# Optimization experiments

Measured on AMD Instinct MI355X. Metric: run time of the kernel, lower is better.

Reference implementation:

```python
import jax, jax.numpy as jnp
import numpy as np

BS, N, C_IMG, C_PT, H, W = 8, 100000, 512, 256, 48, 160


def setup_inputs() -> dict:
    key = jax.random.key(0)
    ks = jax.random.split(key, 8)
    point_feat = jax.random.normal(ks[0], (N, C_PT), dtype=jnp.float32)
    # pillar centers in LiDAR frame: x forward [10,60], y left [-10,10], z [-2,1]
    u = jax.random.uniform(ks[1], (N, 3), dtype=jnp.float32)
    pillar_centers = jnp.stack([
        10.0 + 50.0 * u[:, 0],
        -10.0 + 20.0 * u[:, 1],
        -2.0 + 3.0 * u[:, 2],
    ], axis=1)
    batch_idx = jax.random.randint(ks[2], (N,), 0, BS, dtype=jnp.int32)
    img_feat = jax.random.normal(ks[3], (BS, C_IMG, H, W), dtype=jnp.float32)
    # KITTI-style calibration (per batch, small jitter)
    f, cx, cy = 80.0, 80.0, 24.0
    P2_base = np.array([[f, 0, cx, 0], [0, f, cy, 0], [0, 0, 1, 0]], dtype=np.float32)
    Tr_base = np.array([[0, -1, 0, 0], [0, 0, -1, 0], [1, 0, 0, 0], [0, 0, 0, 1]], dtype=np.float32)
    rng = np.random.RandomState(0)
    P2 = np.stack([P2_base + 0.01 * rng.randn(3, 4).astype(np.float32) for _ in range(BS)])
    R0 = np.stack([np.eye(4, dtype=np.float32) for _ in range(BS)])
    Tr = np.stack([Tr_base + 0.001 * rng.randn(4, 4).astype(np.float32) for _ in range(BS)])
    align_w = jax.random.normal(ks[4], (C_PT, C_IMG), dtype=jnp.float32) * 0.02
    align_b = jax.random.normal(ks[5], (C_PT,), dtype=jnp.float32) * 0.02
    return {
        'point_feat': point_feat, 'pillar_centers': pillar_centers,
        'img_feat': img_feat, 'P2': jnp.asarray(P2), 'R0': jnp.asarray(R0),
        'Tr': jnp.asarray(Tr), 'align_w': align_w, 'align_b': align_b,
        'batch_idx': batch_idx, 'img_h': H, 'img_w': W,
    }


def _fuse(point_feat, pillar_centers, img_feat, P2, R0, Tr, align_w, align_b,
          batch_idx, img_h, img_w):
    n = point_feat.shape[0]
    dt = point_feat.dtype
    # --- project_to_image (vectorized over all points via per-point calib gather) ---
    pts_hom = jnp.concatenate([pillar_centers, jnp.ones((n, 1), dtype=dt)], axis=1)  # [N,4]
    pts_cam = jnp.einsum('nij,nj->ni', Tr[batch_idx], pts_hom)    # [N,4]
    pts_rect = jnp.einsum('nij,nj->ni', R0[batch_idx], pts_cam)   # [N,4]
    pts_img = jnp.einsum('nij,nj->ni', P2[batch_idx], pts_rect)   # [N,3]
    depth = jnp.clip(pts_img[:, 2:3], 1e-5, None)
    uv = pts_img[:, :2] / depth
    valid = ((pts_img[:, 2] > 0) & (uv[:, 0] >= 0) & (uv[:, 0] < img_w)
             & (uv[:, 1] >= 0) & (uv[:, 1] < img_h))
    # --- grid_sample bilinear, align_corners=True, padding_mode='zeros' ---
    # grid = 2*uv/(dim-1)-1 with align_corners=True => pixel coords == uv.
    _, C, Hf, Wf = img_feat.shape
    u_, v_ = uv[:, 0], uv[:, 1]
    x0 = jnp.floor(u_); y0 = jnp.floor(v_)
    wx1 = u_ - x0; wx0 = 1.0 - wx1
    wy1 = v_ - y0; wy0 = 1.0 - wy1

    def gather(xi, yi):
        inb = (xi >= 0) & (xi <= Wf - 1) & (yi >= 0) & (yi <= Hf - 1)
        xc = jnp.clip(xi, 0, Wf - 1).astype(jnp.int32)
        yc = jnp.clip(yi, 0, Hf - 1).astype(jnp.int32)
        f = img_feat[batch_idx, :, yc, xc]  # [N,C]
        return f * inb.astype(dt)[:, None]

    sampled = (gather(x0, y0) * (wx0 * wy0)[:, None]
               + gather(x0 + 1, y0) * (wx1 * wy0)[:, None]
               + gather(x0, y0 + 1) * (wx0 * wy1)[:, None]
               + gather(x0 + 1, y0 + 1) * (wx1 * wy1)[:, None])
    sampled = jnp.where(valid[:, None], sampled, jnp.zeros((), dtype=dt))
    # --- align (Linear) + residual add ---
    aligned = sampled @ align_w.T + align_b
    return point_feat + aligned


def reference(point_feat, pillar_centers, img_feat, P2, R0, Tr, align_w, align_b,
              batch_idx, img_h, img_w):
    return _fuse(point_feat, pillar_centers, img_feat, P2, R0, Tr,
                 align_w, align_b, batch_idx, img_h, img_w)
```

## Files before the change

### kernel.cpp

```cpp
#include <hip/hip_runtime.h>

#define C_IMG 512
#define C_PT  256
#define IMG_H 48
#define IMG_W 160
#define HWPIX (IMG_H * IMG_W)

#define MP   64
#define BK   64
#define SPAD 72

typedef short bf16x8 __attribute__((ext_vector_type(8)));
typedef float f32x4  __attribute__((ext_vector_type(4)));
typedef unsigned u32x4 __attribute__((ext_vector_type(4)));

static __device__ __forceinline__ unsigned short f2bf(float f) {
    unsigned u = __float_as_uint(f);
    u += 0x7fffu + ((u >> 16) & 1u);
    return (unsigned short)(u >> 16);
}
static __device__ __forceinline__ unsigned pack2(float lo, float hi) {
    return (unsigned)f2bf(lo) | ((unsigned)f2bf(hi) << 16);
}
static __device__ __forceinline__ unsigned short f2bf_hu(float f) {
    return (unsigned short)((__float_as_uint(f) + 0x8000u) >> 16);
}
static __device__ __forceinline__ unsigned pack2_hu(float lo, float hi) {
    return ((__float_as_uint(lo) + 0x8000u) >> 16)
         | ((__float_as_uint(hi) + 0x8000u) & 0xffff0000u);
}
static __device__ __forceinline__ float bflo(unsigned v) { return __uint_as_float(v << 16); }
static __device__ __forceinline__ float bfhi(unsigned v) { return __uint_as_float(v & 0xffff0000u); }

__global__ __launch_bounds__(256)
void cvt_w_kernel(const float* __restrict__ alw, unsigned short* __restrict__ alwT) {
    const int i = (blockIdx.x * 256 + threadIdx.x) * 8;
    const float4 a = *(const float4*)(alw + i);
    const float4 b = *(const float4*)(alw + i + 4);
    uint4 o;
    o.x = pack2(a.x, a.y); o.y = pack2(a.z, a.w);
    o.z = pack2(b.x, b.y); o.w = pack2(b.z, b.w);
    *(uint4*)(alwT + i) = o;
}

__global__ __launch_bounds__(256)
void params_kernel(const float* __restrict__ centers,
                   const float* __restrict__ P2,
                   const float* __restrict__ R0,
                   const float* __restrict__ Tr,
                   const int*   __restrict__ bidx,
                   u32x4* __restrict__ poff,
                   f32x4* __restrict__ pwgt,
                   int n)
{
    const int p = blockIdx.x * 256 + threadIdx.x;
    if (p >= n) return;
    const float cx = centers[p * 3 + 0];
    const float cy = centers[p * 3 + 1];
    const float cz = centers[p * 3 + 2];
    const int   b  = bidx[p];
    const float* tr = Tr + b * 16;
    const float c0 = tr[0]*cx + tr[1]*cy + tr[2]*cz + tr[3];
    const float c1 = tr[4]*cx + tr[5]*cy + tr[6]*cz + tr[7];
    const float c2 = tr[8]*cx + tr[9]*cy + tr[10]*cz + tr[11];
    const float c3 = tr[12]*cx + tr[13]*cy + tr[14]*cz + tr[15];
    const float* r0 = R0 + b * 16;
    const float e0 = r0[0]*c0 + r0[1]*c1 + r0[2]*c2 + r0[3]*c3;
    const float e1 = r0[4]*c0 + r0[5]*c1 + r0[6]*c2 + r0[7]*c3;
    const float e2 = r0[8]*c0 + r0[9]*c1 + r0[10]*c2 + r0[11]*c3;
    const float e3 = r0[12]*c0 + r0[13]*c1 + r0[14]*c2 + r0[15]*c3;
    const float* p2 = P2 + b * 12;
    const float ix = p2[0]*e0 + p2[1]*e1 + p2[2]*e2  + p2[3]*e3;
    const float iy = p2[4]*e0 + p2[5]*e1 + p2[6]*e2  + p2[7]*e3;
    const float iz = p2[8]*e0 + p2[9]*e1 + p2[10]*e2 + p2[11]*e3;
    const float depth = fmaxf(iz, 1e-5f);
    const float u = ix / depth;
    const float v = iy / depth;
    const bool valid = (iz > 0.f) && (u >= 0.f) && (u < (float)IMG_W)
                                 && (v >= 0.f) && (v < (float)IMG_H);
    const float x0f = floorf(u), y0f = floorf(v);
    const float wx1 = u - x0f, wx0 = 1.f - wx1;
    const float wy1 = v - y0f, wy0 = 1.f - wy1;
    const float cwv[4] = {wx0 * wy0, wx1 * wy0, wx0 * wy1, wx1 * wy1};
    f32x4 wg; u32x4 of;
    #pragma unroll
    for (int j = 0; j < 4; ++j) {
        const float xf = x0f + (float)(j & 1);
        const float yf = y0f + (float)(j >> 1);
        const bool inb = (xf >= 0.f) && (xf <= (float)(IMG_W - 1))
                      && (yf >= 0.f) && (yf <= (float)(IMG_H - 1));
        const int xc = (int)fminf(fmaxf(xf, 0.f), (float)(IMG_W - 1));
        const int yc = (int)fminf(fmaxf(yf, 0.f), (float)(IMG_H - 1));
        wg[j] = (valid && inb) ? cwv[j] : 0.f;
        of[j] = (unsigned)(((b * IMG_H + yc) * IMG_W + xc) * C_PT);
    }
    poff[p] = of;
    pwgt[p] = wg;
}

__global__ __launch_bounds__(256)
void proj_kernel(const float* __restrict__ img,
                 const unsigned short* __restrict__ wbf,
                 unsigned short* __restrict__ PT)
{
    __shared__ float sF[2][64][68];
    const int blk  = blockIdx.x;
    const int b    = blk / (HWPIX / 64);
    const int hw0  = (blk % (HWPIX / 64)) * 64;
    const int tid  = threadIdx.x;
    const int lane = tid & 63;
    const int wid  = tid >> 6;
    const int l15  = lane & 15;
    const int quad = lane >> 4;

    const int sr   = tid >> 2;
    const int scc  = tid & 3;
    const int sdst = ((scc ^ ((sr >> 3) & 3)) << 4);
    const float* gsrc = img + (size_t)b * C_IMG * HWPIX + hw0 + scc * 16;

    f32x4 acc[4][4];
    #pragma unroll
    for (int i = 0; i < 4; ++i)
        #pragma unroll
        for (int j = 0; j < 4; ++j)
            acc[i][j] = (f32x4){0.f, 0.f, 0.f, 0.f};

    const unsigned short* bw = wbf + (size_t)(wid * 64 + l15) * C_IMG + quad * 8;

    float4 st[4];
    {
        const float* gp = gsrc + (size_t)sr * HWPIX;
        #pragma unroll
        for (int k = 0; k < 4; ++k) st[k] = *(const float4*)(gp + 4 * k);
        #pragma unroll
        for (int k = 0; k < 4; ++k) *(float4*)&sF[0][sr][sdst + 4 * k] = st[k];
    }
    __syncthreads();

    for (int ck = 0; ck < C_IMG / 64; ++ck) {
        const int cur = ck & 1;
        if (ck < C_IMG / 64 - 1) {
            const float* gp = gsrc + (size_t)((ck + 1) * 64 + sr) * HWPIX;
            #pragma unroll
            for (int k = 0; k < 4; ++k) st[k] = *(const float4*)(gp + 4 * k);
        }
        #pragma unroll
        for (int kk = 0; kk < 2; ++kk) {
            bf16x8 af[4], bfr[4];
            #pragma unroll
            for (int nt = 0; nt < 4; ++nt)
                bfr[nt] = *(const bf16x8*)(bw + (size_t)(nt * 16) * C_IMG + ck * 64 + kk * 32);
            const int rbase = kk * 32 + quad * 8;
            #pragma unroll
            for (int mt = 0; mt < 4; ++mt) {
                const int col = ((mt ^ quad) << 4) + l15;
                float f[8];
                #pragma unroll
                for (int j = 0; j < 8; ++j) f[j] = sF[cur][rbase + j][col];
                union { unsigned u[4]; bf16x8 v; } cv;
                #pragma unroll
                for (int w2 = 0; w2 < 4; ++w2)
                    cv.u[w2] = pack2_hu(f[2 * w2], f[2 * w2 + 1]);
                af[mt] = cv.v;
            }
            #pragma unroll
            for (int mt = 0; mt < 4; ++mt)
                #pragma unroll
                for (int nt = 0; nt < 4; ++nt)
                    acc[mt][nt] = __builtin_amdgcn_mfma_f32_16x16x32_bf16(
                        af[mt], bfr[nt], acc[mt][nt], 0, 0, 0);
        }
        if (ck < C_IMG / 64 - 1) {
            #pragma unroll
            for (int k = 0; k < 4; ++k) *(float4*)&sF[cur ^ 1][sr][sdst + 4 * k] = st[k];
        }
        __syncthreads();
    }

    #pragma unroll
    for (int mt = 0; mt < 4; ++mt) {
        #pragma unroll
        for (int r = 0; r < 4; ++r) {
            const int pix = mt * 16 + quad * 4 + r;
            unsigned short* dst = PT + (size_t)(b * HWPIX + hw0 + pix) * C_PT + wid * 64 + l15;
            #pragma unroll
            for (int nt = 0; nt < 4; ++nt)
                dst[nt * 16] = f2bf_hu(acc[mt][nt][r]);
        }
    }
}

__global__ __launch_bounds__(256)
void point_kernel(const float* __restrict__ pf,
                  const unsigned short* __restrict__ PT,
                  const float* __restrict__ alb,
                  const u32x4* __restrict__ poff,
                  const f32x4* __restrict__ pwgt,
                  float* __restrict__ out,
                  int n)
{
    const int tid  = threadIdx.x;
    const int lane = tid & 63;
    const int wid  = tid >> 6;
    const int sub  = lane >> 5;
    const int ch0  = (lane & 31) * 8;
    const int base = blockIdx.x * 32 + wid * 8 + sub;

    const f32x4 ab0 = *(const f32x4*)(alb + ch0);
    const f32x4 ab1 = *(const f32x4*)(alb + ch0 + 4);

    #pragma unroll
    for (int it = 0; it < 4; ++it) {
        const int p = base + it * 2;
        if (p < n) {
            const u32x4 of = poff[p];
            const f32x4 wg = pwgt[p];
            float s0 = 0.f, s1 = 0.f, s2 = 0.f, s3 = 0.f;
            float s4 = 0.f, s5 = 0.f, s6 = 0.f, s7 = 0.f;
            #pragma unroll
            for (int j = 0; j < 4; ++j) {
                const u32x4 g = *(const u32x4*)(PT + of[j] + ch0);
                const float w = wg[j];
                s0 = fmaf(w, bflo(g[0]), s0); s1 = fmaf(w, bfhi(g[0]), s1);
                s2 = fmaf(w, bflo(g[1]), s2); s3 = fmaf(w, bfhi(g[1]), s3);
                s4 = fmaf(w, bflo(g[2]), s4); s5 = fmaf(w, bfhi(g[2]), s5);
                s6 = fmaf(w, bflo(g[3]), s6); s7 = fmaf(w, bfhi(g[3]), s7);
            }
            const size_t idx = (size_t)p * C_PT + ch0;
            const f32x4 a  = __builtin_nontemporal_load((const f32x4*)(pf + idx));
            const f32x4 b4 = __builtin_nontemporal_load((const f32x4*)(pf + idx + 4));
            f32x4 o0, o1;
            o0[0] = a[0] + ab0[0] + s0;  o0[1] = a[1] + ab0[1] + s1;
            o0[2] = a[2] + ab0[2] + s2;  o0[3] = a[3] + ab0[3] + s3;
            o1[0] = b4[0] + ab1[0] + s4; o1[1] = b4[1] + ab1[1] + s5;
            o1[2] = b4[2] + ab1[2] + s6; o1[3] = b4[3] + ab1[3] + s7;
            __builtin_nontemporal_store(o0, (f32x4*)(out + idx));
            __builtin_nontemporal_store(o1, (f32x4*)(out + idx + 4));
        }
    }
}

__global__ __launch_bounds__(256)
void fused_fallback_kernel(const float* __restrict__ pf,
                           const float* __restrict__ centers,
                           const float* __restrict__ img,
                           const float* __restrict__ P2,
                           const float* __restrict__ R0,
                           const float* __restrict__ Tr,
                           const float* __restrict__ alw,
                           const float* __restrict__ alb,
                           const int*   __restrict__ bidx,
                           float* __restrict__ out,
                           int n)
{
    __shared__ float          sWg[MP][4];
    __shared__ int            sOf[MP][4];
    __shared__ unsigned short sS[MP][SPAD];
    __shared__ unsigned short sW[C_PT][SPAD];

    const int tid = threadIdx.x;
    const int pt0 = blockIdx.x * MP;

    if (tid < MP) {
        const int p = pt0 + tid;
        float w[4] = {0.f, 0.f, 0.f, 0.f};
        int   o[4] = {0, 0, 0, 0};
        if (p < n) {
            const float cx = centers[p * 3 + 0];
            const float cy = centers[p * 3 + 1];
            const float cz = centers[p * 3 + 2];
            const int   b  = bidx[p];
            const float* tr = Tr + b * 16;
            const float c0 = tr[0]*cx + tr[1]*cy + tr[2]*cz + tr[3];
            const float c1 = tr[4]*cx + tr[5]*cy + tr[6]*cz + tr[7];
            const float c2 = tr[8]*cx + tr[9]*cy + tr[10]*cz + tr[11];
            const float c3 = tr[12]*cx + tr[13]*cy + tr[14]*cz + tr[15];
            const float* r0 = R0 + b * 16;
            const float e0 = r0[0]*c0 + r0[1]*c1 + r0[2]*c2 + r0[3]*c3;
            const float e1 = r0[4]*c0 + r0[5]*c1 + r0[6]*c2 + r0[7]*c3;
            const float e2 = r0[8]*c0 + r0[9]*c1 + r0[10]*c2 + r0[11]*c3;
            const float e3 = r0[12]*c0 + r0[13]*c1 + r0[14]*c2 + r0[15]*c3;
            const float* p2 = P2 + b * 12;
            const float ix = p2[0]*e0 + p2[1]*e1 + p2[2]*e2  + p2[3]*e3;
            const float iy = p2[4]*e0 + p2[5]*e1 + p2[6]*e2  + p2[7]*e3;
            const float iz = p2[8]*e0 + p2[9]*e1 + p2[10]*e2 + p2[11]*e3;
            const float depth = fmaxf(iz, 1e-5f);
            const float u = ix / depth;
            const float v = iy / depth;
            const bool valid = (iz > 0.f) && (u >= 0.f) && (u < (float)IMG_W)
                                         && (v >= 0.f) && (v < (float)IMG_H);
            const float x0f = floorf(u), y0f = floorf(v);
            const float wx1 = u - x0f, wx0 = 1.f - wx1;
            const float wy1 = v - y0f, wy0 = 1.f - wy1;
            const float cwv[4] = {wx0 * wy0, wx1 * wy0, wx0 * wy1, wx1 * wy1};
            #pragma unroll
            for (int j = 0; j < 4; ++j) {
                const float xf = x0f + (float)(j & 1);
                const float yf = y0f + (float)(j >> 1);
                const bool inb = (xf >= 0.f) && (xf <= (float)(IMG_W - 1))
                              && (yf >= 0.f) && (yf <= (float)(IMG_H - 1));
                const int xc = (int)fminf(fmaxf(xf, 0.f), (float)(IMG_W - 1));
                const int yc = (int)fminf(fmaxf(yf, 0.f), (float)(IMG_H - 1));
                w[j] = (valid && inb) ? cwv[j] : 0.f;
                o[j] = b * C_IMG * HWPIX + yc * IMG_W + xc;
            }
        }
        #pragma unroll
        for (int j = 0; j < 4; ++j) { sWg[tid][j] = w[j]; sOf[tid][j] = o[j]; }
    }

    f32x4 acc[4][4];
    #pragma unroll
    for (int i = 0; i < 4; ++i)
        #pragma unroll
        for (int j = 0; j < 4; ++j)
            acc[i][j] = (f32x4){0.f, 0.f, 0.f, 0.f};

    const int lane = tid & 63;
    const int wid  = tid >> 6;
    const int l15  = lane & 15;
    const int quad = lane >> 4;
    const int sp   = tid >> 2;
    const int ssub = tid & 3;

    __syncthreads();

    for (int ck = 0; ck < C_IMG / BK; ++ck) {
        {
            const float cw0 = sWg[sp][0], cw1 = sWg[sp][1], cw2 = sWg[sp][2], cw3 = sWg[sp][3];
            const int   co0 = sOf[sp][0], co1 = sOf[sp][1], co2 = sOf[sp][2], co3 = sOf[sp][3];
            const int   cb  = ck * BK + ssub * 16;
            const float* ib = img;
            #pragma unroll
            for (int h = 0; h < 2; ++h) {
                uint4 ov;
                unsigned* op = (unsigned*)&ov;
                #pragma unroll
                for (int wI = 0; wI < 4; ++wI) {
                    const int c = cb + h * 8 + 2 * wI;
                    const float vlo = cw0*ib[co0 + c*HWPIX] + cw1*ib[co1 + c*HWPIX]
                                    + cw2*ib[co2 + c*HWPIX] + cw3*ib[co3 + c*HWPIX];
                    const float vhi = cw0*ib[co0 + (c+1)*HWPIX] + cw1*ib[co1 + (c+1)*HWPIX]
                                    + cw2*ib[co2 + (c+1)*HWPIX] + cw3*ib[co3 + (c+1)*HWPIX];
                    op[wI] = pack2(vlo, vhi);
                }
                *(uint4*)&sS[sp][ssub * 16 + h * 8] = ov;
            }
        }
        {
            #pragma unroll
            for (int pass = 0; pass < 4; ++pass) {
                const int r = pass * 64 + (tid >> 2);
                const int c = (tid & 3) * 16;
                const float* wr = alw + (size_t)r * C_IMG + ck * BK + c;
                const float4 f0 = *(const float4*)(wr + 0);
                const float4 f1 = *(const float4*)(wr + 4);
                const float4 f2 = *(const float4*)(wr + 8);
                const float4 f3 = *(const float4*)(wr + 12);
                uint4 oa, ob;
                oa.x = pack2(f0.x, f0.y); oa.y = pack2(f0.z, f0.w);
                oa.z = pack2(f1.x, f1.y); oa.w = pack2(f1.z, f1.w);
                ob.x = pack2(f2.x, f2.y); ob.y = pack2(f2.z, f2.w);
                ob.z = pack2(f3.x, f3.y); ob.w = pack2(f3.z, f3.w);
                *(uint4*)&sW[r][c]     = oa;
                *(uint4*)&sW[r][c + 8] = ob;
            }
        }
        __syncthreads();

        #pragma unroll
        for (int kk = 0; kk < 2; ++kk) {
            bf16x8 af[4], bfr[4];
            #pragma unroll
            for (int mt = 0; mt < 4; ++mt)
                af[mt] = *(const bf16x8*)&sS[mt * 16 + l15][kk * 32 + quad * 8];
            #pragma unroll
            for (int nt = 0; nt < 4; ++nt)
                bfr[nt] = *(const bf16x8*)&sW[wid * 64 + nt * 16 + l15][kk * 32 + quad * 8];
            #pragma unroll
            for (int mt = 0; mt < 4; ++mt)
                #pragma unroll
                for (int nt = 0; nt < 4; ++nt)
                    acc[mt][nt] = __builtin_amdgcn_mfma_f32_16x16x32_bf16(
                        af[mt], bfr[nt], acc[mt][nt], 0, 0, 0);
        }
        __syncthreads();
    }

    #pragma unroll
    for (int mt = 0; mt < 4; ++mt) {
        #pragma unroll
        for (int r = 0; r < 4; ++r) {
            const int p = pt0 + mt * 16 + quad * 4 + r;
            if (p < n) {
                #pragma unroll
                for (int nt = 0; nt < 4; ++nt) {
                    const int nc = wid * 64 + nt * 16 + l15;
                    const size_t idx = (size_t)p * C_PT + nc;
                    out[idx] = pf[idx] + alb[nc] + acc[mt][nt][r];
                }
            }
        }
    }
}

extern "C" void kernel_launch(void* const* d_in, const int* in_sizes, int n_in,
                              void* d_out, int out_size, void* d_ws, size_t ws_size,
                              hipStream_t stream) {
    const float* pf      = (const float*)d_in[0];
    const float* centers = (const float*)d_in[1];
    const float* img     = (const float*)d_in[2];
    const float* P2      = (const float*)d_in[3];
    const float* R0      = (const float*)d_in[4];
    const float* Tr      = (const float*)d_in[5];
    const float* alw     = (const float*)d_in[6];
    const float* alb     = (const float*)d_in[7];
    const int*   bidx    = (const int*)d_in[8];
    float*       out     = (float*)d_out;

    const int n  = in_sizes[8];
    const int bs = in_sizes[3] / 12;

    const size_t tpt = (size_t)bs * HWPIX * C_PT * sizeof(unsigned short);
    const size_t tw  = (size_t)C_PT * C_IMG * sizeof(unsigned short);
    const size_t tof = (size_t)n * 16;
    const size_t twg = (size_t)n * 16;
    if (ws_size >= tpt + tw + tof + twg) {
        unsigned short* PT  = (unsigned short*)d_ws;
        unsigned short* wbf = (unsigned short*)((char*)d_ws + tpt);
        u32x4*          poff = (u32x4*)((char*)d_ws + tpt + tw);
        f32x4*          pwgt = (f32x4*)((char*)d_ws + tpt + tw + tof);

        cvt_w_kernel<<<(C_PT * C_IMG / 8) / 256, 256, 0, stream>>>(alw, wbf);
        params_kernel<<<(n + 255) / 256, 256, 0, stream>>>(
            centers, P2, R0, Tr, bidx, poff, pwgt, n);
        proj_kernel<<<bs * (HWPIX / 64), 256, 0, stream>>>(img, wbf, PT);
        point_kernel<<<(n + 31) / 32, 256, 0, stream>>>(
            pf, PT, alb, poff, pwgt, out, n);
    } else {
        const int nblk = (n + MP - 1) / MP;
        fused_fallback_kernel<<<nblk, 256, 0, stream>>>(
            pf, centers, img, P2, R0, Tr, alw, alb, bidx, out, n);
    }
}
```

Before: 334.8 us.

## Merge prep kernels, stage image tile as bf16 in LDS, batch point gathers

Three changes. The weight conversion and per-point parameter kernels become one launch, split by block index. The projection GEMM now converts image features to packed bf16 pairs when writing them to shared memory, using an XOR-swizzled layout, so each MFMA A-fragment is one 16-byte LDS read instead of eight scalar float reads plus packing. The point kernel assigns four consecutive points per half-wave and issues all 16 gathers and the residual loads before any arithmetic, which raises memory-level parallelism at the cost of more registers.

```diff
diff --git a/kernel.cpp b/kernel.cpp
--- a/kernel.cpp
+++ b/kernel.cpp
@@ -33,26 +33,27 @@
 static __device__ __forceinline__ float bfhi(unsigned v) { return __uint_as_float(v & 0xffff0000u); }
 
 __global__ __launch_bounds__(256)
-void cvt_w_kernel(const float* __restrict__ alw, unsigned short* __restrict__ alwT) {
-    const int i = (blockIdx.x * 256 + threadIdx.x) * 8;
-    const float4 a = *(const float4*)(alw + i);
-    const float4 b = *(const float4*)(alw + i + 4);
-    uint4 o;
-    o.x = pack2(a.x, a.y); o.y = pack2(a.z, a.w);
-    o.z = pack2(b.x, b.y); o.w = pack2(b.z, b.w);
-    *(uint4*)(alwT + i) = o;
-}
-
-__global__ __launch_bounds__(256)
-void params_kernel(const float* __restrict__ centers,
-                   const float* __restrict__ P2,
-                   const float* __restrict__ R0,
-                   const float* __restrict__ Tr,
-                   const int*   __restrict__ bidx,
-                   u32x4* __restrict__ poff,
-                   f32x4* __restrict__ pwgt,
-                   int n)
+void prep_kernel(const float* __restrict__ centers,
+                 const float* __restrict__ P2,
+                 const float* __restrict__ R0,
+                 const float* __restrict__ Tr,
+                 const int*   __restrict__ bidx,
+                 const float* __restrict__ alw,
+                 u32x4* __restrict__ poff,
+                 f32x4* __restrict__ pwgt,
+                 unsigned short* __restrict__ wbf,
+                 int n, int nParamBlk)
 {
+    if ((int)blockIdx.x >= nParamBlk) {
+        const int i = (((int)blockIdx.x - nParamBlk) * 256 + (int)threadIdx.x) * 8;
+        const float4 a = *(const float4*)(alw + i);
+        const float4 b = *(const float4*)(alw + i + 4);
+        uint4 o;
+        o.x = pack2(a.x, a.y); o.y = pack2(a.z, a.w);
+        o.z = pack2(b.x, b.y); o.w = pack2(b.z, b.w);
+        *(uint4*)(wbf + i) = o;
+        return;
+    }
     const int p = blockIdx.x * 256 + threadIdx.x;
     if (p >= n) return;
     const float cx = centers[p * 3 + 0];
@@ -103,7 +104,7 @@
                  const unsigned short* __restrict__ wbf,
                  unsigned short* __restrict__ PT)
 {
-    __shared__ float sF[2][64][68];
+    __shared__ unsigned sT[2][64][32];
     const int blk  = blockIdx.x;
     const int b    = blk / (HWPIX / 64);
     const int hw0  = (blk % (HWPIX / 64)) * 64;
@@ -113,10 +114,9 @@
     const int l15  = lane & 15;
     const int quad = lane >> 4;
 
-    const int sr   = tid >> 2;
-    const int scc  = tid & 3;
-    const int sdst = ((scc ^ ((sr >> 3) & 3)) << 4);
-    const float* gsrc = img + (size_t)b * C_IMG * HWPIX + hw0 + scc * 16;
+    const int g   = tid >> 3;
+    const int sub = tid & 7;
+    const float* gA = img + (size_t)b * C_IMG * HWPIX + (size_t)(2 * g) * HWPIX + hw0 + sub * 8;
 
     f32x4 acc[4][4];
     #pragma unroll
@@ -127,41 +127,47 @@
 
     const unsigned short* bw = wbf + (size_t)(wid * 64 + l15) * C_IMG + quad * 8;
 
-    float4 st[4];
-    {
-        const float* gp = gsrc + (size_t)sr * HWPIX;
-        #pragma unroll
-        for (int k = 0; k < 4; ++k) st[k] = *(const float4*)(gp + 4 * k);
-        #pragma unroll
-        for (int k = 0; k < 4; ++k) *(float4*)&sF[0][sr][sdst + 4 * k] = st[k];
-    }
+    f32x4 fa0, fa1, fb0, fb1;
+    #define STAGE_LOAD(CK) do {                                                     \
+        const float* pA = gA + (size_t)((CK) * 64) * HWPIX;                         \
+        const float* pB = pA + HWPIX;                                               \
+        fa0 = __builtin_nontemporal_load((const f32x4*)pA);                         \
+        fa1 = __builtin_nontemporal_load((const f32x4*)(pA + 4));                   \
+        fb0 = __builtin_nontemporal_load((const f32x4*)pB);                         \
+        fb1 = __builtin_nontemporal_load((const f32x4*)(pB + 4));                   \
+    } while (0)
+    #define STAGE_COMMIT(BUF) do {                                                 \
+        _Pragma("unroll")                                                          \
+        for (int i = 0; i < 4; ++i) {                                              \
+            const int chk = ((g >> 2) ^ i ^ sub) & 7;                              \
+            sT[BUF][sub * 8 + i][(chk << 2) | (g & 3)] = pack2_hu(fa0[i], fb0[i]); \
+        }                                                                          \
+        _Pragma("unroll")                                                          \
+        for (int i = 0; i < 4; ++i) {                                              \
+            const int chk = ((g >> 2) ^ (i + 4) ^ sub) & 7;                        \
+            sT[BUF][sub * 8 + i + 4][(chk << 2) | (g & 3)] = pack2_hu(fa1[i], fb1[i]); \
+        }                                                                          \
+    } while (0)
+
+    STAGE_LOAD(0);
+    STAGE_COMMIT(0);
     __syncthreads();
 
     for (int ck = 0; ck < C_IMG / 64; ++ck) {
         const int cur = ck & 1;
-        if (ck < C_IMG / 64 - 1) {
-            const float* gp = gsrc + (size_t)((ck + 1) * 64 + sr) * HWPIX;
-            #pragma unroll
-            for (int k = 0; k < 4; ++k) st[k] = *(const float4*)(gp + 4 * k);
-        }
+        if (ck < C_IMG / 64 - 1) STAGE_LOAD(ck + 1);
+
         #pragma unroll
         for (int kk = 0; kk < 2; ++kk) {
             bf16x8 af[4], bfr[4];
             #pragma unroll
             for (int nt = 0; nt < 4; ++nt)
                 bfr[nt] = *(const bf16x8*)(bw + (size_t)(nt * 16) * C_IMG + ck * 64 + kk * 32);
-            const int rbase = kk * 32 + quad * 8;
             #pragma unroll
             for (int mt = 0; mt < 4; ++mt) {
-                const int col = ((mt ^ quad) << 4) + l15;
-                float f[8];
-                #pragma unroll
-                for (int j = 0; j < 8; ++j) f[j] = sF[cur][rbase + j][col];
-                union { unsigned u[4]; bf16x8 v; } cv;
-                #pragma unroll
-                for (int w2 = 0; w2 < 4; ++w2)
-                    cv.u[w2] = pack2_hu(f[2 * w2], f[2 * w2 + 1]);
-                af[mt] = cv.v;
+                const int px  = mt * 16 + l15;
+                const int chk = ((kk * 4 + quad) ^ (px & 7) ^ ((px >> 3) & 7)) & 7;
+                af[mt] = *(const bf16x8*)&sT[cur][px][chk << 2];
             }
             #pragma unroll
             for (int mt = 0; mt < 4; ++mt)
@@ -170,12 +176,11 @@
                     acc[mt][nt] = __builtin_amdgcn_mfma_f32_16x16x32_bf16(
                         af[mt], bfr[nt], acc[mt][nt], 0, 0, 0);
         }
-        if (ck < C_IMG / 64 - 1) {
-            #pragma unroll
-            for (int k = 0; k < 4; ++k) *(float4*)&sF[cur ^ 1][sr][sdst + 4 * k] = st[k];
-        }
+        if (ck < C_IMG / 64 - 1) STAGE_COMMIT(cur ^ 1);
         __syncthreads();
     }
+    #undef STAGE_LOAD
+    #undef STAGE_COMMIT
 
     #pragma unroll
     for (int mt = 0; mt < 4; ++mt) {
@@ -200,40 +205,55 @@
                   int n)
 {
     const int tid  = threadIdx.x;
-    const int lane = tid & 63;
-    const int wid  = tid >> 6;
-    const int sub  = lane >> 5;
-    const int ch0  = (lane & 31) * 8;
-    const int base = blockIdx.x * 32 + wid * 8 + sub;
+    const int half = tid >> 5;
+    const int ch0  = (tid & 31) * 8;
+    const int p0   = blockIdx.x * 32 + half * 4;
 
     const f32x4 ab0 = *(const f32x4*)(alb + ch0);
     const f32x4 ab1 = *(const f32x4*)(alb + ch0 + 4);
 
+    u32x4 of[4]; f32x4 wg[4];
     #pragma unroll
     for (int it = 0; it < 4; ++it) {
-        const int p = base + it * 2;
-        if (p < n) {
-            const u32x4 of = poff[p];
-            const f32x4 wg = pwgt[p];
+        const int p = min(p0 + it, n - 1);
+        of[it] = poff[p];
+        wg[it] = pwgt[p];
+    }
+    u32x4 gv[4][4];
+    #pragma unroll
+    for (int it = 0; it < 4; ++it)
+        #pragma unroll
+        for (int j = 0; j < 4; ++j)
+            gv[it][j] = *(const u32x4*)(PT + of[it][j] + ch0);
+
+    f32x4 pa[4], pb[4];
+    #pragma unroll
+    for (int it = 0; it < 4; ++it) {
+        const size_t idx = (size_t)min(p0 + it, n - 1) * C_PT + ch0;
+        pa[it] = __builtin_nontemporal_load((const f32x4*)(pf + idx));
+        pb[it] = __builtin_nontemporal_load((const f32x4*)(pf + idx + 4));
+    }
+
+    #pragma unroll
+    for (int it = 0; it < 4; ++it) {
+        if (p0 + it < n) {
             float s0 = 0.f, s1 = 0.f, s2 = 0.f, s3 = 0.f;
             float s4 = 0.f, s5 = 0.f, s6 = 0.f, s7 = 0.f;
             #pragma unroll
             for (int j = 0; j < 4; ++j) {
-                const u32x4 g = *(const u32x4*)(PT + of[j] + ch0);
-                const float w = wg[j];
-                s0 = fmaf(w, bflo(g[0]), s0); s1 = fmaf(w, bfhi(g[0]), s1);
-                s2 = fmaf(w, bflo(g[1]), s2); s3 = fmaf(w, bfhi(g[1]), s3);
-                s4 = fmaf(w, bflo(g[2]), s4); s5 = fmaf(w, bfhi(g[2]), s5);
-                s6 = fmaf(w, bflo(g[3]), s6); s7 = fmaf(w, bfhi(g[3]), s7);
-            }
-            const size_t idx = (size_t)p * C_PT + ch0;
-            const f32x4 a  = __builtin_nontemporal_load((const f32x4*)(pf + idx));
-            const f32x4 b4 = __builtin_nontemporal_load((const f32x4*)(pf + idx + 4));
+                const u32x4 gq = gv[it][j];
+                const float w = wg[it][j];
+                s0 = fmaf(w, bflo(gq[0]), s0); s1 = fmaf(w, bfhi(gq[0]), s1);
+                s2 = fmaf(w, bflo(gq[1]), s2); s3 = fmaf(w, bfhi(gq[1]), s3);
+                s4 = fmaf(w, bflo(gq[2]), s4); s5 = fmaf(w, bfhi(gq[2]), s5);
+                s6 = fmaf(w, bflo(gq[3]), s6); s7 = fmaf(w, bfhi(gq[3]), s7);
+            }
+            const size_t idx = (size_t)(p0 + it) * C_PT + ch0;
             f32x4 o0, o1;
-            o0[0] = a[0] + ab0[0] + s0;  o0[1] = a[1] + ab0[1] + s1;
-            o0[2] = a[2] + ab0[2] + s2;  o0[3] = a[3] + ab0[3] + s3;
-            o1[0] = b4[0] + ab1[0] + s4; o1[1] = b4[1] + ab1[1] + s5;
-            o1[2] = b4[2] + ab1[2] + s6; o1[3] = b4[3] + ab1[3] + s7;
+            o0[0] = pa[it][0] + ab0[0] + s0;  o0[1] = pa[it][1] + ab0[1] + s1;
+            o0[2] = pa[it][2] + ab0[2] + s2;  o0[3] = pa[it][3] + ab0[3] + s3;
+            o1[0] = pb[it][0] + ab1[0] + s4;  o1[1] = pb[it][1] + ab1[1] + s5;
+            o1[2] = pb[it][2] + ab1[2] + s6;  o1[3] = pb[it][3] + ab1[3] + s7;
             __builtin_nontemporal_store(o0, (f32x4*)(out + idx));
             __builtin_nontemporal_store(o1, (f32x4*)(out + idx + 4));
         }
@@ -431,9 +451,10 @@
         u32x4*          poff = (u32x4*)((char*)d_ws + tpt + tw);
         f32x4*          pwgt = (f32x4*)((char*)d_ws + tpt + tw + tof);
 
-        cvt_w_kernel<<<(C_PT * C_IMG / 8) / 256, 256, 0, stream>>>(alw, wbf);
-        params_kernel<<<(n + 255) / 256, 256, 0, stream>>>(
-            centers, P2, R0, Tr, bidx, poff, pwgt, n);
+        const int npb = (n + 255) / 256;
+        const int ncb = (C_PT * C_IMG / 8) / 256;
+        prep_kernel<<<npb + ncb, 256, 0, stream>>>(
+            centers, P2, R0, Tr, bidx, alw, poff, pwgt, wbf, n, npb);
         proj_kernel<<<bs * (HWPIX / 64), 256, 0, stream>>>(img, wbf, PT);
         point_kernel<<<(n + 31) / 32, 256, 0, stream>>>(
             pf, PT, alb, poff, pwgt, out, n);
```

Measured after the change: 337.9 us. About the same (+0.9%).
